# Kernel tuning notes

Hardware: AMD Instinct MI355X
Metric: run time of the kernel (lower is better)

## Reference

```python
import jax, jax.numpy as jnp
import numpy as np
from jax import lax

N, C = 32768, 128
K5, K3 = 125, 27
EPS = 1e-5


def sparse_conv(feats, nbr, W):
    """Gather-GEMM-accumulate sparse conv.
    feats: [N, Cin]; nbr: [K, N] int (neighbor row per kernel tap); W: [K, Cin, Cout].
    out[i] = sum_k feats[nbr[k, i]] @ W[k]
    """
    def step(acc, kw):
        idx, Wk = kw
        return acc + feats[idx] @ Wk, None
    acc0 = jnp.zeros((feats.shape[0], W.shape[-1]), feats.dtype)
    acc, _ = lax.scan(step, acc0, (nbr, W))
    return acc


def batchnorm(x, gamma, beta):
    mu = jnp.mean(x, axis=0)
    var = jnp.mean(jnp.square(x - mu), axis=0)
    return (x - mu) * lax.rsqrt(var + EPS) * gamma + beta


def setup_inputs() -> dict:
    key = jax.random.key(0)
    ks = jax.random.split(key, 12)
    s1 = 1.0 / np.sqrt(C)            # 1x1 conv fan-in
    s5 = 1.0 / np.sqrt(C * K5)       # 5^3 conv fan-in
    s3 = 1.0 / np.sqrt(C * K3)       # 3^3 conv fan-in
    return {
        "x": jax.random.normal(ks[0], (N, C), jnp.float32),
        "Wa1": jax.random.normal(ks[1], (C, C), jnp.float32) * s1,
        "Wv1": jax.random.normal(ks[2], (C, C), jnp.float32) * s1,
        "W5": jax.random.normal(ks[3], (K5, C, C), jnp.float32) * s5,
        "W31": jax.random.normal(ks[4], (K3, C, C), jnp.float32) * s3,
        "W32": jax.random.normal(ks[5], (K3, C, C), jnp.float32) * s3,
        "gamma1": jnp.ones((C,), jnp.float32),
        "beta1": jnp.zeros((C,), jnp.float32),
        "gamma2": jnp.ones((C,), jnp.float32),
        "beta2": jnp.zeros((C,), jnp.float32),
        "nbr5": jax.random.randint(ks[6], (N, K5), 0, N, jnp.int32),
        "nbr3a": jax.random.randint(ks[7], (N, K3), 0, N, jnp.int32),
        "nbr3b": jax.random.randint(ks[8], (N, K3), 0, N, jnp.int32),
    }


def reference(x, Wa1, Wv1, W5, W31, W32, gamma1, beta1, gamma2, beta2, nbr5, nbr3a, nbr3b):
    residual = x
    # a branch: 1x1 conv (stride=1 -> kernel_size 1) then 5^3 sparse conv
    a = x @ Wa1
    a = sparse_conv(a, nbr5.T, W5)
    # v branch: 1x1 conv
    v = x @ Wv1
    # gated elementwise mult
    out = a * v
    # conv1 -> BN1 -> (dropout=identity) + residual
    out = sparse_conv(out, nbr3a.T, W31)
    out = batchnorm(out, gamma1, beta1)
    out = out + residual
    residual = out
    out = jax.nn.relu(out)
    # conv2 -> BN2 -> (dropout=identity) + residual -> relu
    out = sparse_conv(out, nbr3b.T, W32)
    out = batchnorm(out, gamma2, beta2)
    out = out + residual
    out = jax.nn.relu(out)
    return out
```

## Files before the change

kernel.cpp:

```cpp
#include <hip/hip_runtime.h>
#include <stdint.h>


#define NPTS 32768
#define C 128
#define EPS 1e-5f

typedef unsigned short u16;
using bfrag = __attribute__((ext_vector_type(8))) short;
using f32x4 = __attribute__((ext_vector_type(4))) float;

__device__ __forceinline__ float b2f(u16 u) {
  union { unsigned int i; float f; } x;
  x.i = ((unsigned int)u) << 16;
  return x.f;
}
__device__ __forceinline__ u16 f2b(float f) {
  union { float f; unsigned int i; } x;
  x.f = f;
  unsigned int r = x.i + 0x7FFFu + ((x.i >> 16) & 1u);
  return (u16)(r >> 16);
}

__device__ __forceinline__ void g2l16(const void* g, void* l) {
  __builtin_amdgcn_global_load_lds(
      (const __attribute__((address_space(1))) unsigned int*)g,
      (__attribute__((address_space(3))) unsigned int*)l,
      16, 0, 0);
}

#define GG_W(N)                                                            \
  asm volatile("s_waitcnt vmcnt(" #N ")" ::: "memory");                    \
  __builtin_amdgcn_sched_barrier(0)

#define GG_WB(N)                                                           \
  asm volatile("s_waitcnt vmcnt(" #N ") lgkmcnt(0)" ::: "memory");         \
  __builtin_amdgcn_s_barrier();                                            \
  __builtin_amdgcn_sched_barrier(0)

template <int NTAPS, int EPI>
__global__ __launch_bounds__(512, 1)
void gg_kernel(const u16* __restrict__ src, const u16* __restrict__ WT,
               const int* __restrict__ nbr, u16* __restrict__ outb,
               float* __restrict__ outf, const u16* __restrict__ vmul) {
  __shared__ uint4 lds[8192];
  char* const base = (char*)lds;
  char* const bufs[4] = {base, base + 32768, base + 65536, base + 98304};

  const int tid  = threadIdx.x;
  const int lane = tid & 63;
  const int wv   = tid >> 6;
  const int wq   = wv & 3;
  const int wr   = wq >> 1, wc = wq & 1;
  const int kk2w = wv >> 2;
  const int lsub = lane >> 4, lm = lane & 15;
  const int r8   = lane >> 3;
  const int cs8  = lane & 7;
  const int row0 = blockIdx.x * 128;

  f32x4 acc[4][4];
#pragma unroll
  for (int i = 0; i < 4; i++)
#pragma unroll
    for (int j = 0; j < 4; j++) acc[i][j] = (f32x4)(0.0f);

  auto loadIdx = [&](int (&d)[2], int st) {
    const int tp = st < NTAPS ? st : st - NTAPS;
#pragma unroll
    for (int j = 0; j < 2; j++) {
      const int gr = row0 + wv * 16 + j * 8 + r8;
      const int* p = nbr + (size_t)gr * NTAPS + tp;
      asm volatile("global_load_dword %0, %1, off"
                   : "=v"(d[j]) : "v"(p) : "memory");
    }
  };

  auto stageA = [&](char* buf, const int (&id)[2], int st) {
    const int h = st < NTAPS ? 0 : 1;
#pragma unroll
    for (int j = 0; j < 2; j++) {
      const char* gp = (const char*)src + ((size_t)(unsigned)id[j] << 8)
                     + (h << 7) + ((cs8 ^ r8) << 4);
      g2l16(gp, buf + (wv * 16 + j * 8) * 128);
    }
  };

  auto stageB = [&](char* buf, int st) {
    const int tp = st < NTAPS ? st : st - NTAPS;
    const int h = st < NTAPS ? 0 : 1;
    const char* wt = (const char*)WT + ((size_t)tp << 15) + (h << 7);
#pragma unroll
    for (int j = 0; j < 2; j++) {
      const int col = wv * 16 + j * 8 + r8;
      g2l16(wt + ((size_t)col << 8) + ((cs8 ^ r8) << 4),
            buf + 16384 + (wv * 16 + j * 8) * 128);
    }
  };

  auto computeS = [&](const char* buf) {
    bfrag af[4], bg[4];
#pragma unroll
    for (int rt = 0; rt < 4; rt++) {
      const int row = wr * 64 + rt * 16 + lm;
      af[rt] = *(const bfrag*)(buf + row * 128
                               + (((kk2w * 4 + lsub) ^ (row & 7)) << 4));
    }
#pragma unroll
    for (int ct = 0; ct < 4; ct++) {
      const int col = wc * 64 + ct * 16 + lm;
      bg[ct] = *(const bfrag*)(buf + 16384 + col * 128
                               + (((kk2w * 4 + lsub) ^ (col & 7)) << 4));
    }
    __builtin_amdgcn_s_setprio(1);
#pragma unroll
    for (int rt = 0; rt < 4; rt++)
#pragma unroll
      for (int ct = 0; ct < 4; ct++)
        acc[rt][ct] = __builtin_amdgcn_mfma_f32_16x16x32_bf16(
            af[rt], bg[ct], acc[rt][ct], 0, 0, 0);
    __builtin_amdgcn_s_setprio(0);
  };

  if constexpr (NTAPS == 1) {
    int idv[2];
#pragma unroll
    for (int j = 0; j < 2; j++) idv[j] = row0 + wv * 16 + j * 8 + r8;
    stageA(bufs[0], idv, 0); stageB(bufs[0], 0);
    stageA(bufs[1], idv, 1); stageB(bufs[1], 1);
    GG_WB(0);
    computeS(bufs[0]);
    computeS(bufs[1]);
  } else {
    constexpr int S = 2 * NTAPS;
    int idr[4][2], ip0[2], ip1[2], ip2[2];
    loadIdx(ip0, 0); loadIdx(ip1, 1); loadIdx(ip2, 2);
    GG_W(0);
    stageA(bufs[0], ip0, 0); stageB(bufs[0], 0); loadIdx(idr[1], 3);
    stageA(bufs[1], ip1, 1); stageB(bufs[1], 1); loadIdx(idr[2], 4);
    stageA(bufs[2], ip2, 2); stageB(bufs[2], 2); loadIdx(idr[3], 5);

#define GG_SUB(p)                                                          \
    GG_WB(12);                                                             \
    stageA(bufs[((p) + 3) & 3], idr[((p) + 1) & 3], s + (p) + 3);          \
    stageB(bufs[((p) + 3) & 3], s + (p) + 3);                              \
    loadIdx(idr[(p) & 3], s + (p) + 6);                                    \
    computeS(bufs[(p) & 3]);

#pragma unroll 1
    for (int s = 0; s < S - 6; s += 4) {
      GG_SUB(0)
      GG_SUB(1)
      GG_SUB(2)
      GG_SUB(3)
    }
#undef GG_SUB

    GG_WB(12);
    stageA(bufs[3], idr[1], S - 3); stageB(bufs[3], S - 3);
    computeS(bufs[0]);
    GG_WB(10);
    stageA(bufs[0], idr[2], S - 2); stageB(bufs[0], S - 2);
    computeS(bufs[1]);
    GG_WB(8);
    stageA(bufs[1], idr[3], S - 1); stageB(bufs[1], S - 1);
    computeS(bufs[2]);
    GG_WB(8);
    computeS(bufs[3]);
    GG_WB(4);
    computeS(bufs[0]);
    GG_WB(0);
    computeS(bufs[1]);
  }

  asm volatile("s_waitcnt lgkmcnt(0)" ::: "memory");
  __builtin_amdgcn_s_barrier();
  __builtin_amdgcn_sched_barrier(0);
  if (wv >= 4) {
    char* dst = base + (size_t)(wv - 4) * 16384 + lane * 16;
#pragma unroll
    for (int rt = 0; rt < 4; rt++)
#pragma unroll
      for (int ct = 0; ct < 4; ct++)
        *(f32x4*)(dst + (rt * 4 + ct) * 1024) = acc[rt][ct];
  }
  asm volatile("s_waitcnt lgkmcnt(0)" ::: "memory");
  __builtin_amdgcn_s_barrier();
  __builtin_amdgcn_sched_barrier(0);

  if (wv < 4) {
    const char* psrc = base + (size_t)wv * 16384 + lane * 16;
#pragma unroll
    for (int rt = 0; rt < 4; rt++) {
      const int rowb = row0 + wr * 64 + rt * 16 + lsub * 4;
#pragma unroll
      for (int ct = 0; ct < 4; ct++) {
        const f32x4 part = *(const f32x4*)(psrc + (rt * 4 + ct) * 1024);
        const f32x4 v4 = acc[rt][ct] + part;
        const int c = wc * 64 + ct * 16 + lm;
#pragma unroll
        for (int reg = 0; reg < 4; reg++) {
          const size_t off = (size_t)(rowb + reg) * C + c;
          const float v = v4[reg];
          if (EPI == 0)      outb[off] = f2b(v);
          else if (EPI == 1) outb[off] = f2b(v * b2f(vmul[off]));
          else               outf[off] = v;
        }
      }
    }
  }
}

__global__ __launch_bounds__(256)
void cvt_kernel(const float* __restrict__ x, u16* __restrict__ xb) {
  const int i = (blockIdx.x * 256 + threadIdx.x) * 4;
  const float4 v = *(const float4*)(x + i);
  ushort4 o;
  o.x = f2b(v.x); o.y = f2b(v.y); o.z = f2b(v.z); o.w = f2b(v.w);
  *(ushort4*)(xb + i) = o;
}

__global__ __launch_bounds__(256)
void wt_kernel(const float* __restrict__ W5, const float* __restrict__ W31,
               const float* __restrict__ W32, const float* __restrict__ Wa1,
               const float* __restrict__ Wv1,
               u16* __restrict__ T5, u16* __restrict__ T31, u16* __restrict__ T32,
               u16* __restrict__ Ta1, u16* __restrict__ Tv1) {
  const int b = blockIdx.x;
  const float* w;
  u16* o;
  if (b < 125)       { w = W5  + (size_t)b * 16384;         o = T5  + (size_t)b * 16384; }
  else if (b < 152)  { w = W31 + (size_t)(b - 125) * 16384; o = T31 + (size_t)(b - 125) * 16384; }
  else if (b < 179)  { w = W32 + (size_t)(b - 152) * 16384; o = T32 + (size_t)(b - 152) * 16384; }
  else if (b == 179) { w = Wa1; o = Ta1; }
  else               { w = Wv1; o = Tv1; }
  __shared__ u16 tile[128 * 129];
  for (int i = threadIdx.x; i < C * C; i += 256)
    tile[(i & 127) * 129 + (i >> 7)] = f2b(w[i]);
  __syncthreads();
  for (int i = threadIdx.x; i < C * C; i += 256)
    o[i] = tile[(i >> 7) * 129 + (i & 127)];
}

__global__ __launch_bounds__(256)
void bnp_kernel(const float* __restrict__ t, float* __restrict__ psum,
                float* __restrict__ psq) {
  const int b = blockIdx.x;
  const int c = threadIdx.x & 127;
  const int h = threadIdx.x >> 7;
  const float* p = t + (size_t)(b * 128 + h * 64) * C + c;
  float s = 0.f, q = 0.f;
#pragma unroll 8
  for (int j = 0; j < 64; j++) {
    const float v = p[(size_t)j * C];
    s += v; q += v * v;
  }
  __shared__ float ls[256], lq[256];
  ls[threadIdx.x] = s; lq[threadIdx.x] = q;
  __syncthreads();
  if (h == 0) {
    psum[b * 128 + c] = ls[c] + ls[c + 128];
    psq[b * 128 + c]  = lq[c] + lq[c + 128];
  }
}

__global__ __launch_bounds__(256)
void bnfin_kernel(const float* __restrict__ psum, const float* __restrict__ psq,
                  const float* __restrict__ gamma, const float* __restrict__ beta,
                  float* __restrict__ scale, float* __restrict__ shift) {
  const int c = blockIdx.x;
  const int t = threadIdx.x;
  float s = psum[(size_t)t * 128 + c];
  float q = psq[(size_t)t * 128 + c];
#pragma unroll
  for (int o = 32; o > 0; o >>= 1) {
    s += __shfl_down(s, o);
    q += __shfl_down(q, o);
  }
  __shared__ float ls[4], lq[4];
  if ((t & 63) == 0) { ls[t >> 6] = s; lq[t >> 6] = q; }
  __syncthreads();
  if (t == 0) {
    s = ls[0] + ls[1] + ls[2] + ls[3];
    q = lq[0] + lq[1] + lq[2] + lq[3];
    const float mean = s * (1.0f / NPTS);
    const float var  = q * (1.0f / NPTS) - mean * mean;
    const float sc   = rsqrtf(var + EPS) * gamma[c];
    scale[c] = sc;
    shift[c] = beta[c] - mean * sc;
  }
}

__global__ __launch_bounds__(256)
void ew1_kernel(const float* __restrict__ t, const float* __restrict__ x,
                const float* __restrict__ scale, const float* __restrict__ shift,
                u16* __restrict__ res, u16* __restrict__ h) {
  const int i = blockIdx.x * 256 + threadIdx.x;
  const int c = i & 127;
  const float o = t[i] * scale[c] + shift[c] + x[i];
  res[i] = f2b(o);
  h[i] = f2b(o < 0.f ? 0.f : o);
}

__global__ __launch_bounds__(256)
void ew2_kernel(const float* __restrict__ t2, const u16* __restrict__ res,
                const float* __restrict__ scale, const float* __restrict__ shift,
                float* __restrict__ y) {
  const int i = blockIdx.x * 256 + threadIdx.x;
  const int c = i & 127;
  const float o = t2[i] * scale[c] + shift[c] + b2f(res[i]);
  y[i] = o < 0.f ? 0.f : o;
}

extern "C" void kernel_launch(void* const* d_in, const int* in_sizes, int n_in,
                              void* d_out, int out_size, void* d_ws, size_t ws_size,
                              hipStream_t stream) {
  (void)in_sizes; (void)n_in; (void)out_size; (void)ws_size;

  const float* x   = (const float*)d_in[0];
  const float* Wa1 = (const float*)d_in[1];
  const float* Wv1 = (const float*)d_in[2];
  const float* W5  = (const float*)d_in[3];
  const float* W31 = (const float*)d_in[4];
  const float* W32 = (const float*)d_in[5];
  const float* g1  = (const float*)d_in[6];
  const float* b1  = (const float*)d_in[7];
  const float* g2  = (const float*)d_in[8];
  const float* b2  = (const float*)d_in[9];
  const int* nbr5  = (const int*)d_in[10];
  const int* nbr3a = (const int*)d_in[11];
  const int* nbr3b = (const int*)d_in[12];

  char* w = (char*)d_ws;
  u16* WT5  = (u16*)w; w += 4096000;
  u16* WT31 = (u16*)w; w += 884736;
  u16* WT32 = (u16*)w; w += 884736;
  u16* WTa1 = (u16*)w; w += 32768;
  u16* WTv1 = (u16*)w; w += 32768;
  char* AV  = w;       w += 16777216;
  u16*   a_b = (u16*)AV;
  u16*   v_b = (u16*)(AV + 8388608);
  float* tf  = (float*)AV;
  u16* g_b  = (u16*)w; w += 8388608;
  u16* h_b  = (u16*)w; w += 8388608;
  u16* xb   = h_b;
  float* psum = (float*)w; w += 131072;
  float* psq  = (float*)w; w += 131072;
  float* sc1  = (float*)w; w += 512;
  float* sh1  = (float*)w; w += 512;
  float* sc2  = (float*)w; w += 512;
  float* sh2  = (float*)w; w += 512;

  const dim3 B512(512), GG(NPTS / 128), B256(256), GBN(256), GEW(NPTS * C / 256);
  float* yout = (float*)d_out;

  cvt_kernel<<<dim3(NPTS * C / 1024), B256, 0, stream>>>(x, xb);
  wt_kernel<<<dim3(181), B256, 0, stream>>>(W5, W31, W32, Wa1, Wv1,
                                            WT5, WT31, WT32, WTa1, WTv1);

  gg_kernel<1, 0><<<GG, B512, 0, stream>>>(xb, WTa1, nullptr, a_b, nullptr, nullptr);
  gg_kernel<1, 0><<<GG, B512, 0, stream>>>(xb, WTv1, nullptr, v_b, nullptr, nullptr);

  gg_kernel<125, 1><<<GG, B512, 0, stream>>>(a_b, WT5, nbr5, g_b, nullptr, v_b);

  gg_kernel<27, 2><<<GG, B512, 0, stream>>>(g_b, WT31, nbr3a, nullptr, tf, nullptr);
  bnp_kernel<<<GBN, B256, 0, stream>>>(tf, psum, psq);
  bnfin_kernel<<<dim3(128), B256, 0, stream>>>(psum, psq, g1, b1, sc1, sh1);
  ew1_kernel<<<GEW, B256, 0, stream>>>(tf, x, sc1, sh1, g_b, h_b);

  gg_kernel<27, 2><<<GG, B512, 0, stream>>>(h_b, WT32, nbr3b, nullptr, tf, nullptr);
  bnp_kernel<<<GBN, B256, 0, stream>>>(tf, psum, psq);
  bnfin_kernel<<<dim3(128), B256, 0, stream>>>(psum, psq, g2, b2, sc2, sh2);
  ew2_kernel<<<GEW, B256, 0, stream>>>(tf, g_b, sc2, sh2, yout);
}
```

Before: 372.2 us.

## Stage full-tap tiles with double buffering and fuse BN partial sums into GEMM

The gather-GEMM pipeline now stages the whole 128-channel K-slice of a tap at once in two 64KB buffers, replacing the four-deep pipeline over half-taps. This halves the number of barrier/stage steps but gives a shallower prefetch depth. Separately, the BN partial sum and sum-of-squares are computed in the fp32 epilogue of the 27-tap convs via shuffles and LDS, which removes the separate bnp_kernel pass that re-reads the fp32 output.

```diff
diff --git a/kernel.cpp b/kernel.cpp
--- a/kernel.cpp
+++ b/kernel.cpp
@@ -42,10 +42,12 @@
 __global__ __launch_bounds__(512, 1)
 void gg_kernel(const u16* __restrict__ src, const u16* __restrict__ WT,
                const int* __restrict__ nbr, u16* __restrict__ outb,
-               float* __restrict__ outf, const u16* __restrict__ vmul) {
+               float* __restrict__ outf, const u16* __restrict__ vmul,
+               float* __restrict__ psum, float* __restrict__ psq) {
   __shared__ uint4 lds[8192];
   char* const base = (char*)lds;
-  char* const bufs[4] = {base, base + 32768, base + 65536, base + 98304};
+  char* const b0 = base;
+  char* const b1 = base + 65536;
 
   const int tid  = threadIdx.x;
   const int lane = tid & 63;
@@ -64,8 +66,7 @@
 #pragma unroll
     for (int j = 0; j < 4; j++) acc[i][j] = (f32x4)(0.0f);
 
-  auto loadIdx = [&](int (&d)[2], int st) {
-    const int tp = st < NTAPS ? st : st - NTAPS;
+  auto loadIdx = [&](int (&d)[2], int tp) {
 #pragma unroll
     for (int j = 0; j < 2; j++) {
       const int gr = row0 + wv * 16 + j * 8 + r8;
@@ -75,101 +76,89 @@
     }
   };
 
-  auto stageA = [&](char* buf, const int (&id)[2], int st) {
-    const int h = st < NTAPS ? 0 : 1;
+  auto stageT = [&](char* buf, const int (&id)[2], int tp) {
+    const char* wt = (const char*)WT + ((size_t)tp << 15);
 #pragma unroll
     for (int j = 0; j < 2; j++) {
-      const char* gp = (const char*)src + ((size_t)(unsigned)id[j] << 8)
-                     + (h << 7) + ((cs8 ^ r8) << 4);
-      g2l16(gp, buf + (wv * 16 + j * 8) * 128);
-    }
-  };
-
-  auto stageB = [&](char* buf, int st) {
-    const int tp = st < NTAPS ? st : st - NTAPS;
-    const int h = st < NTAPS ? 0 : 1;
-    const char* wt = (const char*)WT + ((size_t)tp << 15) + (h << 7);
+      const char* ga = (const char*)src + ((size_t)(unsigned)id[j] << 8)
+                     + ((cs8 ^ r8) << 4);
+#pragma unroll
+      for (int h = 0; h < 2; h++)
+        g2l16(ga + (h << 7), buf + h * 16384 + (wv * 16 + j * 8) * 128);
+    }
 #pragma unroll
     for (int j = 0; j < 2; j++) {
       const int col = wv * 16 + j * 8 + r8;
-      g2l16(wt + ((size_t)col << 8) + ((cs8 ^ r8) << 4),
-            buf + 16384 + (wv * 16 + j * 8) * 128);
+      const char* gb = wt + ((size_t)col << 8) + ((cs8 ^ r8) << 4);
+#pragma unroll
+      for (int h = 0; h < 2; h++)
+        g2l16(gb + (h << 7), buf + 32768 + h * 16384 + (wv * 16 + j * 8) * 128);
     }
   };
 
-  auto computeS = [&](const char* buf) {
-    bfrag af[4], bg[4];
-#pragma unroll
-    for (int rt = 0; rt < 4; rt++) {
-      const int row = wr * 64 + rt * 16 + lm;
-      af[rt] = *(const bfrag*)(buf + row * 128
-                               + (((kk2w * 4 + lsub) ^ (row & 7)) << 4));
-    }
-#pragma unroll
-    for (int ct = 0; ct < 4; ct++) {
-      const int col = wc * 64 + ct * 16 + lm;
-      bg[ct] = *(const bfrag*)(buf + 16384 + col * 128
-                               + (((kk2w * 4 + lsub) ^ (col & 7)) << 4));
-    }
-    __builtin_amdgcn_s_setprio(1);
-#pragma unroll
-    for (int rt = 0; rt < 4; rt++)
-#pragma unroll
-      for (int ct = 0; ct < 4; ct++)
-        acc[rt][ct] = __builtin_amdgcn_mfma_f32_16x16x32_bf16(
-            af[rt], bg[ct], acc[rt][ct], 0, 0, 0);
-    __builtin_amdgcn_s_setprio(0);
+  auto computeF = [&](const char* buf) {
+    const char* Ah = buf + kk2w * 16384;
+    const char* Bh = buf + 32768 + kk2w * 16384;
+#pragma unroll
+    for (int kx = 0; kx < 2; kx++) {
+      bfrag af[4], bg[4];
+#pragma unroll
+      for (int rt = 0; rt < 4; rt++) {
+        const int row = wr * 64 + rt * 16 + lm;
+        af[rt] = *(const bfrag*)(Ah + row * 128
+                                 + (((kx * 4 + lsub) ^ (row & 7)) << 4));
+      }
+#pragma unroll
+      for (int ct = 0; ct < 4; ct++) {
+        const int col = wc * 64 + ct * 16 + lm;
+        bg[ct] = *(const bfrag*)(Bh + col * 128
+                                 + (((kx * 4 + lsub) ^ (col & 7)) << 4));
+      }
+      __builtin_amdgcn_s_setprio(1);
+#pragma unroll
+      for (int rt = 0; rt < 4; rt++)
+#pragma unroll
+        for (int ct = 0; ct < 4; ct++)
+          acc[rt][ct] = __builtin_amdgcn_mfma_f32_16x16x32_bf16(
+              af[rt], bg[ct], acc[rt][ct], 0, 0, 0);
+      __builtin_amdgcn_s_setprio(0);
+    }
   };
 
   if constexpr (NTAPS == 1) {
     int idv[2];
 #pragma unroll
     for (int j = 0; j < 2; j++) idv[j] = row0 + wv * 16 + j * 8 + r8;
-    stageA(bufs[0], idv, 0); stageB(bufs[0], 0);
-    stageA(bufs[1], idv, 1); stageB(bufs[1], 1);
+    stageT(b0, idv, 0);
     GG_WB(0);
-    computeS(bufs[0]);
-    computeS(bufs[1]);
+    computeF(b0);
   } else {
-    constexpr int S = 2 * NTAPS;
-    int idr[4][2], ip0[2], ip1[2], ip2[2];
-    loadIdx(ip0, 0); loadIdx(ip1, 1); loadIdx(ip2, 2);
+    int idT[2], idO[2], idE[2];
+    loadIdx(idT, 0);
     GG_W(0);
-    stageA(bufs[0], ip0, 0); stageB(bufs[0], 0); loadIdx(idr[1], 3);
-    stageA(bufs[1], ip1, 1); stageB(bufs[1], 1); loadIdx(idr[2], 4);
-    stageA(bufs[2], ip2, 2); stageB(bufs[2], 2); loadIdx(idr[3], 5);
-
-#define GG_SUB(p)                                                          \
-    GG_WB(12);                                                             \
-    stageA(bufs[((p) + 3) & 3], idr[((p) + 1) & 3], s + (p) + 3);          \
-    stageB(bufs[((p) + 3) & 3], s + (p) + 3);                              \
-    loadIdx(idr[(p) & 3], s + (p) + 6);                                    \
-    computeS(bufs[(p) & 3]);
+    stageT(b0, idT, 0);
+    loadIdx(idO, 1);
+    loadIdx(idE, 2);
 
 #pragma unroll 1
-    for (int s = 0; s < S - 6; s += 4) {
-      GG_SUB(0)
-      GG_SUB(1)
-      GG_SUB(2)
-      GG_SUB(3)
-    }
-#undef GG_SUB
-
-    GG_WB(12);
-    stageA(bufs[3], idr[1], S - 3); stageB(bufs[3], S - 3);
-    computeS(bufs[0]);
-    GG_WB(10);
-    stageA(bufs[0], idr[2], S - 2); stageB(bufs[0], S - 2);
-    computeS(bufs[1]);
-    GG_WB(8);
-    stageA(bufs[1], idr[3], S - 1); stageB(bufs[1], S - 1);
-    computeS(bufs[2]);
-    GG_WB(8);
-    computeS(bufs[3]);
-    GG_WB(4);
-    computeS(bufs[0]);
+    for (int t = 0; t < NTAPS - 3; t += 2) {
+      GG_WB(2);
+      stageT(b1, idO, t + 1);
+      loadIdx(idO, t + 3);
+      computeF(b0);
+      GG_WB(2);
+      stageT(b0, idE, t + 2);
+      loadIdx(idE, t + 4);
+      computeF(b1);
+    }
+    GG_WB(2);
+    stageT(b1, idO, NTAPS - 2);
+    computeF(b0);
     GG_WB(0);
-    computeS(bufs[1]);
+    stageT(b0, idE, NTAPS - 1);
+    computeF(b1);
+    GG_WB(0);
+    computeF(b0);
   }
 
   asm volatile("s_waitcnt lgkmcnt(0)" ::: "memory");
@@ -189,6 +178,7 @@
 
   if (wv < 4) {
     const char* psrc = base + (size_t)wv * 16384 + lane * 16;
+    float bs[4] = {0.f, 0.f, 0.f, 0.f}, bq[4] = {0.f, 0.f, 0.f, 0.f};
 #pragma unroll
     for (int rt = 0; rt < 4; rt++) {
       const int rowb = row0 + wr * 64 + rt * 16 + lsub * 4;
@@ -203,9 +193,39 @@
           const float v = v4[reg];
           if (EPI == 0)      outb[off] = f2b(v);
           else if (EPI == 1) outb[off] = f2b(v * b2f(vmul[off]));
-          else               outf[off] = v;
+          else {
+            outf[off] = v;
+            bs[ct] += v;
+            bq[ct] += v * v;
+          }
         }
       }
+    }
+    if (EPI == 2) {
+      float* Sa = (float*)(base + 65536);
+#pragma unroll
+      for (int ct = 0; ct < 4; ct++) {
+        float s = bs[ct], q = bq[ct];
+        s += __shfl_xor(s, 16); q += __shfl_xor(q, 16);
+        s += __shfl_xor(s, 32); q += __shfl_xor(q, 32);
+        if (lsub == 0) {
+          Sa[wv * 64 + ct * 16 + lm]       = s;
+          Sa[256 + wv * 64 + ct * 16 + lm] = q;
+        }
+      }
+    }
+  }
+  if (EPI == 2) {
+    asm volatile("s_waitcnt lgkmcnt(0)" ::: "memory");
+    __builtin_amdgcn_s_barrier();
+    __builtin_amdgcn_sched_barrier(0);
+    if (tid < 128) {
+      const float* Sa = (const float*)(base + 65536);
+      const int hi = tid >> 6, lo = tid & 63;
+      psum[(size_t)blockIdx.x * 128 + tid] =
+          Sa[hi * 64 + lo] + Sa[(hi + 2) * 64 + lo];
+      psq[(size_t)blockIdx.x * 128 + tid] =
+          Sa[256 + hi * 64 + lo] + Sa[256 + (hi + 2) * 64 + lo];
     }
   }
 }
@@ -242,28 +262,6 @@
 }
 
 __global__ __launch_bounds__(256)
-void bnp_kernel(const float* __restrict__ t, float* __restrict__ psum,
-                float* __restrict__ psq) {
-  const int b = blockIdx.x;
-  const int c = threadIdx.x & 127;
-  const int h = threadIdx.x >> 7;
-  const float* p = t + (size_t)(b * 128 + h * 64) * C + c;
-  float s = 0.f, q = 0.f;
-#pragma unroll 8
-  for (int j = 0; j < 64; j++) {
-    const float v = p[(size_t)j * C];
-    s += v; q += v * v;
-  }
-  __shared__ float ls[256], lq[256];
-  ls[threadIdx.x] = s; lq[threadIdx.x] = q;
-  __syncthreads();
-  if (h == 0) {
-    psum[b * 128 + c] = ls[c] + ls[c + 128];
-    psq[b * 128 + c]  = lq[c] + lq[c + 128];
-  }
-}
-
-__global__ __launch_bounds__(256)
 void bnfin_kernel(const float* __restrict__ psum, const float* __restrict__ psq,
                   const float* __restrict__ gamma, const float* __restrict__ beta,
                   float* __restrict__ scale, float* __restrict__ shift) {
@@ -350,25 +348,23 @@
   float* sc2  = (float*)w; w += 512;
   float* sh2  = (float*)w; w += 512;
 
-  const dim3 B512(512), GG(NPTS / 128), B256(256), GBN(256), GEW(NPTS * C / 256);
+  const dim3 B512(512), GG(NPTS / 128), B256(256), GEW(NPTS * C / 256);
   float* yout = (float*)d_out;
 
   cvt_kernel<<<dim3(NPTS * C / 1024), B256, 0, stream>>>(x, xb);
   wt_kernel<<<dim3(181), B256, 0, stream>>>(W5, W31, W32, Wa1, Wv1,
                                             WT5, WT31, WT32, WTa1, WTv1);
 
-  gg_kernel<1, 0><<<GG, B512, 0, stream>>>(xb, WTa1, nullptr, a_b, nullptr, nullptr);
-  gg_kernel<1, 0><<<GG, B512, 0, stream>>>(xb, WTv1, nullptr, v_b, nullptr, nullptr);
-
-  gg_kernel<125, 1><<<GG, B512, 0, stream>>>(a_b, WT5, nbr5, g_b, nullptr, v_b);
-
-  gg_kernel<27, 2><<<GG, B512, 0, stream>>>(g_b, WT31, nbr3a, nullptr, tf, nullptr);
-  bnp_kernel<<<GBN, B256, 0, stream>>>(tf, psum, psq);
+  gg_kernel<1, 0><<<GG, B512, 0, stream>>>(xb, WTa1, nullptr, a_b, nullptr, nullptr, nullptr, nullptr);
+  gg_kernel<1, 0><<<GG, B512, 0, stream>>>(xb, WTv1, nullptr, v_b, nullptr, nullptr, nullptr, nullptr);
+
+  gg_kernel<125, 1><<<GG, B512, 0, stream>>>(a_b, WT5, nbr5, g_b, nullptr, v_b, nullptr, nullptr);
+
+  gg_kernel<27, 2><<<GG, B512, 0, stream>>>(g_b, WT31, nbr3a, nullptr, tf, nullptr, psum, psq);
   bnfin_kernel<<<dim3(128), B256, 0, stream>>>(psum, psq, g1, b1, sc1, sh1);
   ew1_kernel<<<GEW, B256, 0, stream>>>(tf, x, sc1, sh1, g_b, h_b);
 
-  gg_kernel<27, 2><<<GG, B512, 0, stream>>>(h_b, WT32, nbr3b, nullptr, tf, nullptr);
-  bnp_kernel<<<GBN, B256, 0, stream>>>(tf, psum, psq);
+  gg_kernel<27, 2><<<GG, B512, 0, stream>>>(h_b, WT32, nbr3b, nullptr, tf, nullptr, psum, psq);
   bnfin_kernel<<<dim3(128), B256, 0, stream>>>(psum, psq, g2, b2, sc2, sh2);
   ew2_kernel<<<GEW, B256, 0, stream>>>(tf, g_b, sc2, sh2, yout);
 }
```

New measurement: 382.7 us. 2.8% more time.
